# Performance work log

Measured on AMD Instinct MI355X. Metric: run time of the kernel, lower is better.

The kernel has to match this reference:

```python
import jax, jax.numpy as jnp
import numpy as np

BS, C_IN, L = 64, 64, 4096
C_OUT, KS, K, RATIO = 128, 7, 4, 4
HIDDEN = C_IN // RATIO
PAD, TEMP = 3, 30.0


def setup_inputs() -> dict:
    key = jax.random.key(0)
    k1, k2, k3, k4, k5 = jax.random.split(key, 5)
    x = jax.random.normal(k1, (BS, C_IN, L), dtype=jnp.float32)
    # attention 1x1 convs stored as matmul matrices
    w_attn1 = jax.random.normal(k2, (HIDDEN, C_IN), dtype=jnp.float32) * (2.0 / C_IN) ** 0.5
    w_attn2 = jax.random.normal(k3, (K, HIDDEN), dtype=jnp.float32) * (2.0 / HIDDEN) ** 0.5
    # K-bank conv weights [K, out, in, ks] and biases [K, out]
    weight = jax.random.normal(k4, (K, C_OUT, C_IN, KS), dtype=jnp.float32) * 0.05
    bias = jax.random.normal(k5, (K, C_OUT), dtype=jnp.float32) * 0.05
    return {"x": x, "w_attn1": w_attn1, "w_attn2": w_attn2, "weight": weight, "bias": bias}


def reference(x, w_attn1, w_attn2, weight, bias):
    # Attention1d: global avg pool -> 1x1 conv -> relu -> 1x1 conv -> softmax(./T)
    pooled = jnp.mean(x, axis=-1)                      # [bs, C_in]
    h = jax.nn.relu(pooled @ w_attn1.T)                # [bs, hidden]
    logits = h @ w_attn2.T                             # [bs, K]
    att = jax.nn.softmax(logits / TEMP, axis=-1)       # [bs, K]

    # softmax-weighted aggregation of the K weight banks -> per-sample kernels
    agg_w = jnp.einsum('bk,koif->boif', att, weight)   # [bs, out, in, ks]
    agg_b = att @ bias                                 # [bs, out]

    # per-sample conv1d (the grouped-conv trick), vectorized with vmap
    def conv_one(xi, wi):
        # xi: [C_in, L], wi: [out, in, ks]
        return jax.lax.conv_general_dilated(
            xi[None], wi, window_strides=(1,), padding=[(PAD, PAD)],
            dimension_numbers=('NCH', 'OIH', 'NCH'))[0]  # [out, L]

    out = jax.vmap(conv_one)(x, agg_w) + agg_b[:, :, None]  # [bs, out, L]
    return out
```

## Files before the change

### kernel.cpp

```cpp
#include <hip/hip_runtime.h>

typedef __bf16 bf16;
typedef __bf16 bf16x8 __attribute__((ext_vector_type(8)));
typedef __bf16 bf16x2 __attribute__((ext_vector_type(2)));
typedef float f32x4 __attribute__((ext_vector_type(4)));

#define BS 64
#define CI 64
#define LEN 4096
#define CO 128
#define KS 7
#define NK 4
#define HID 16
#define TEMP 30.0f

#define KTOT 448
#define WROW 456
#define WBAT (CO * WROW)
#define LTILE 128
#define TPB 8
#define XB_ROWS 4112
#define XB_ELE (XB_ROWS * 64)

__device__ __forceinline__ void gl_lds16(const void* g, void* l) {
    auto gp = reinterpret_cast<const __attribute__((address_space(1))) unsigned int*>(
        reinterpret_cast<unsigned long long>(g));
    auto lp = reinterpret_cast<__attribute__((address_space(3))) unsigned int*>(
        reinterpret_cast<unsigned long long>(l));
    __builtin_amdgcn_global_load_lds(gp, lp, 16, 0, 0);
}

__global__ __launch_bounds__(256) void trans_kernel(const float* __restrict__ x,
                                                    bf16* __restrict__ xbf,
                                                    float* __restrict__ part) {
    int bid = blockIdx.x;
    int b = bid >> 3, lt = bid & 7;
    int t = threadIdx.x;
    int si = t >> 2, sf = t & 3;
    __shared__ __align__(16) bf16 lds_t[128 * 72];
    __shared__ float lds_red[64 * 4];

    const float* xb = x + (size_t)b * CI * LEN;
    bf16* xo = xbf + (size_t)b * XB_ELE;
    float psum = 0.f;

    for (int st = 0; st < 4; ++st) {
        int ls = lt * 512 + st * 128;
        float4 v[8];
#pragma unroll
        for (int j = 0; j < 8; ++j)
            v[j] = *(const float4*)(xb + (size_t)si * LEN + ls + 4 * (sf + 4 * j));
#pragma unroll
        for (int j = 0; j < 8; ++j) {
            psum += (v[j].x + v[j].y) + (v[j].z + v[j].w);
#pragma unroll
            for (int e = 0; e < 4; ++e)
                lds_t[(4 * (sf + 4 * j) + e) * 72 + si] = (bf16)((&v[j].x)[e]);
        }
        __syncthreads();
        int row = t >> 4, l16 = t & 15;
#pragma unroll
        for (int pass = 0; pass < 8; ++pass) {
            int r = pass * 16 + row;
            int gl = ls + r + 8;
            uint2 d = *(const uint2*)(lds_t + r * 72 + l16 * 4);
            int c = l16 >> 1;
            int sw = c ^ (gl & 7);
            *(uint2*)((char*)xo + (size_t)gl * 128 + sw * 16 + (l16 & 1) * 8) = d;
        }
        __syncthreads();
    }

    lds_red[si * 4 + sf] = psum;
    __syncthreads();
    if (t < 64)
        part[((size_t)b * 8 + lt) * 64 + t] =
            lds_red[t * 4] + lds_red[t * 4 + 1] + lds_red[t * 4 + 2] + lds_red[t * 4 + 3];

    if (lt == 0 && t < 128) *(uint2*)((char*)xo + t * 8) = make_uint2(0u, 0u);
    if (lt == 7 && t < 128) *(uint2*)((char*)xo + (size_t)4104 * 128 + t * 8) = make_uint2(0u, 0u);
}

__global__ void aggw_kernel(const float* __restrict__ part,
                            const float* __restrict__ w1,
                            const float* __restrict__ w2,
                            const float* __restrict__ weight,
                            float* __restrict__ att_g,
                            bf16* __restrict__ wagg) {
    int o = blockIdx.x >> 1;
    int bh = blockIdx.x & 1;
    int t = threadIdx.x;
    __shared__ float p[32 * 64];
    __shared__ float hsh[32 * 16];
    __shared__ float att_s[32][4];
    __shared__ float lw[4 * KTOT];

    const float* wo = weight + (size_t)o * KTOT;
    for (int idx = t; idx < 4 * KTOT; idx += 256) {
        int bank = idx / KTOT;
        int r = idx - bank * KTOT;
        lw[idx] = wo[(size_t)bank * (CO * KTOT) + r];
    }
    for (int idx = t; idx < 32 * 64; idx += 256) {
        int bb = idx >> 6, i = idx & 63;
        const float* pp = part + ((size_t)(bh * 32 + bb) * 8) * 64 + i;
        float s = 0.f;
#pragma unroll
        for (int j = 0; j < 8; ++j) s += pp[j * 64];
        p[idx] = s * (1.0f / LEN);
    }
    __syncthreads();

    {
        int bb = t >> 3, h2 = (t & 7) * 2;
#pragma unroll
        for (int u = 0; u < 2; ++u) {
            int hh = h2 + u;
            float s = 0.f;
            for (int i = 0; i < 64; ++i) s += p[bb * 64 + i] * w1[hh * 64 + i];
            hsh[bb * 16 + hh] = fmaxf(s, 0.f);
        }
    }
    __syncthreads();
    if (t < 32) {
        float lg[NK], m = -1e30f;
#pragma unroll
        for (int k = 0; k < NK; ++k) {
            float s = 0.f;
            for (int j = 0; j < HID; ++j) s += hsh[t * 16 + j] * w2[k * HID + j];
            lg[k] = s * (1.0f / TEMP);
            m = fmaxf(m, lg[k]);
        }
        float e[NK], tot = 0.f;
#pragma unroll
        for (int k = 0; k < NK; ++k) { e[k] = expf(lg[k] - m); tot += e[k]; }
        float inv = 1.0f / tot;
#pragma unroll
        for (int k = 0; k < NK; ++k) {
            att_s[t][k] = e[k] * inv;
            if (blockIdx.x < 2) att_g[(bh * 32 + t) * NK + k] = e[k] * inv;
        }
    }
    __syncthreads();

    if (t < 224) {
        float w8[8];
#pragma unroll
        for (int j = 0; j < 2; ++j) {
            int kout = 2 * t + j;
            int i = kout & 63, f = kout >> 6;
#pragma unroll
            for (int bank = 0; bank < 4; ++bank)
                w8[j * 4 + bank] = lw[bank * KTOT + i * KS + f];
        }
        for (int bb = 0; bb < 32; ++bb) {
            int b = bh * 32 + bb;
            float a0 = att_s[bb][0], a1 = att_s[bb][1];
            float a2 = att_s[bb][2], a3 = att_s[bb][3];
            float v0 = a0 * w8[0] + a1 * w8[1] + a2 * w8[2] + a3 * w8[3];
            float v1 = a0 * w8[4] + a1 * w8[5] + a2 * w8[6] + a3 * w8[7];
            bf16x2 pk; pk[0] = (bf16)v0; pk[1] = (bf16)v1;
            *(bf16x2*)(wagg + (size_t)b * WBAT + o * WROW + 2 * t) = pk;
        }
    }
}

__global__ __launch_bounds__(256, 2) void conv_kernel(
    const bf16* __restrict__ xbf,
    const bf16* __restrict__ wagg,
    const float* __restrict__ att_g,
    const float* __restrict__ bias,
    float* __restrict__ out) {
    __shared__ __align__(1024) bf16 lds_x[2][144 * 64];
    __shared__ float aggb_l[CO];

    int nwg = gridDim.x;
    int bid = blockIdx.x;
    int logical = (bid & 7) * (nwg >> 3) + (bid >> 3);
    int b = logical >> 3;
    int rem = logical & 7;
    int oh = rem >> 2, lsp = rem & 3;

    int t = threadIdx.x;
    int lane = t & 63, wid = t >> 6;
    int ln = lane & 15, g = lane >> 4;
    int wm = wid >> 1, wn = wid & 1;

    if (t < CO) {
        float a0 = att_g[b * NK + 0], a1 = att_g[b * NK + 1];
        float a2 = att_g[b * NK + 2], a3 = att_g[b * NK + 3];
        aggb_l[t] = a0 * bias[0 * CO + t] + a1 * bias[1 * CO + t] +
                    a2 * bias[2 * CO + t] + a3 * bias[3 * CO + t];
    }

    const bf16* wgb = wagg + (size_t)b * WBAT
                    + (size_t)(oh * 64 + wm * 32 + ln) * WROW + g * 8;
    bf16x8 av[2][14];
#pragma unroll
    for (int mf = 0; mf < 2; ++mf)
#pragma unroll
        for (int kk = 0; kk < 14; ++kk)
            av[mf][kk] = *(const bf16x8*)(wgb + mf * 16 * WROW + kk * 32);

    int l0base = lsp * (LTILE * TPB);
    const bf16* xb = xbf + (size_t)b * XB_ELE;

    auto stage = [&](int buf, int l0) {
        const char* src = (const char*)xb + (size_t)l0 * 128 + lane * 16;
        char* dst = (char*)lds_x[buf];
        for (int c = wid; c < 18; c += 4)
            gl_lds16(src + c * 1024, dst + c * 1024);
    };

    stage(0, l0base);
    __syncthreads();

    float bias_r[2][4];
    int orow_off[2][4];
#pragma unroll
    for (int mf = 0; mf < 2; ++mf)
#pragma unroll
        for (int r = 0; r < 4; ++r) {
            int o = oh * 64 + wm * 32 + mf * 16 + g * 4 + r;
            bias_r[mf][r] = aggb_l[o];
            orow_off[mf][r] = (b * CO + o) * LEN;
        }

    int prow = wn * 64 + ln + 5;

    for (int tl = 0; tl < TPB; ++tl) {
        int l0 = l0base + tl * LTILE;
        if (tl + 1 < TPB) stage((tl + 1) & 1, l0 + LTILE);

        f32x4 acc[2][4];
#pragma unroll
        for (int mf = 0; mf < 2; ++mf)
#pragma unroll
            for (int nf = 0; nf < 4; ++nf)
                acc[mf][nf] = (f32x4){0.f, 0.f, 0.f, 0.f};

        const char* lb = (const char*)lds_x[tl & 1];

#pragma unroll
        for (int kk = 0; kk < 14; ++kk) {
            int f = kk >> 1;
            int key = (prow + f) & 7;
            int swz = (((kk & 1) * 4 + g) ^ key) * 16;
            bf16x8 bv[4];
#pragma unroll
            for (int nf = 0; nf < 4; ++nf)
                bv[nf] = *(const bf16x8*)(lb + (prow + nf * 16 + f) * 128 + swz);
#pragma unroll
            for (int mf = 0; mf < 2; ++mf)
#pragma unroll
                for (int nf = 0; nf < 4; ++nf)
                    acc[mf][nf] = __builtin_amdgcn_mfma_f32_16x16x32_bf16(
                        av[mf][kk], bv[nf], acc[mf][nf], 0, 0, 0);
        }

        if (tl + 1 < TPB) __syncthreads();

#pragma unroll
        for (int mf = 0; mf < 2; ++mf)
#pragma unroll
            for (int nf = 0; nf < 4; ++nf) {
                int l = l0 + wn * 64 + nf * 16 + ln;
#pragma unroll
                for (int r = 0; r < 4; ++r)
                    out[(size_t)orow_off[mf][r] + l] = acc[mf][nf][r] + bias_r[mf][r];
            }
    }
}

extern "C" void kernel_launch(void* const* d_in, const int* in_sizes, int n_in,
                              void* d_out, int out_size, void* d_ws, size_t ws_size,
                              hipStream_t stream) {
    const float* x  = (const float*)d_in[0];
    const float* w1 = (const float*)d_in[1];
    const float* w2 = (const float*)d_in[2];
    const float* wt = (const float*)d_in[3];
    const float* bs = (const float*)d_in[4];
    float* out = (float*)d_out;

    bf16* xbf    = (bf16*)d_ws;
    bf16* wagg   = (bf16*)((char*)d_ws + (size_t)BS * XB_ELE * 2);
    float* part  = (float*)((char*)wagg + (size_t)BS * WBAT * 2);
    float* att_g = part + BS * 8 * 64;

    trans_kernel<<<BS * 8, 256, 0, stream>>>(x, xbf, part);
    aggw_kernel<<<CO * 2, 256, 0, stream>>>(part, w1, w2, wt, att_g, wagg);
    conv_kernel<<<BS * 8, 256, 0, stream>>>(xbf, wagg, att_g, bs, out);
}
```

Before: 66.06 us.

## Split transpose kernel into more blocks, prefetch both tiles, widen LDS/global stores

The transpose/cast kernel now runs 16 blocks per sample instead of 8, each handling 256 columns. Both 128-column tiles are loaded into registers up front so the global reads overlap, and the LDS-to-global copy uses 16-byte vectors instead of 8-byte ones. The trailing barrier is dropped on the last tile, and the partial-sum buffer and the reduction in the aggregation kernel grow to 16 parts. The aim is more memory-level parallelism and occupancy in this bandwidth-bound pre-pass, at the cost of higher register pressure from holding 16 float4 values per thread.

Measured after the change: 66.85 us. Within noise of the previous version (+1.2%).

```diff
diff --git a/kernel.cpp b/kernel.cpp
--- a/kernel.cpp
+++ b/kernel.cpp
@@ -21,6 +21,7 @@
 #define TPB 8
 #define XB_ROWS 4112
 #define XB_ELE (XB_ROWS * 64)
+#define NPART 16
 
 __device__ __forceinline__ void gl_lds16(const void* g, void* l) {
     auto gp = reinterpret_cast<const __attribute__((address_space(1))) unsigned int*>(
@@ -34,7 +35,7 @@
                                                     bf16* __restrict__ xbf,
                                                     float* __restrict__ part) {
     int bid = blockIdx.x;
-    int b = bid >> 3, lt = bid & 7;
+    int b = bid >> 4, lt = bid & 15;
     int t = threadIdx.x;
     int si = t >> 2, sf = t & 3;
     __shared__ __align__(16) bf16 lds_t[128 * 72];
@@ -43,42 +44,49 @@
     const float* xb = x + (size_t)b * CI * LEN;
     bf16* xo = xbf + (size_t)b * XB_ELE;
     float psum = 0.f;
-
-    for (int st = 0; st < 4; ++st) {
-        int ls = lt * 512 + st * 128;
-        float4 v[8];
-#pragma unroll
-        for (int j = 0; j < 8; ++j)
-            v[j] = *(const float4*)(xb + (size_t)si * LEN + ls + 4 * (sf + 4 * j));
+    int ls0 = lt * 256;
+
+    float4 v0[8], v1[8];
+#pragma unroll
+    for (int j = 0; j < 8; ++j)
+        v0[j] = *(const float4*)(xb + (size_t)si * LEN + ls0 + 4 * (sf + 4 * j));
+#pragma unroll
+    for (int j = 0; j < 8; ++j)
+        v1[j] = *(const float4*)(xb + (size_t)si * LEN + ls0 + 128 + 4 * (sf + 4 * j));
+
+#pragma unroll
+    for (int st = 0; st < 2; ++st) {
+        const float4* v = st ? v1 : v0;
+        int ls = ls0 + st * 128;
 #pragma unroll
         for (int j = 0; j < 8; ++j) {
-            psum += (v[j].x + v[j].y) + (v[j].z + v[j].w);
+            float4 vv = v[j];
+            psum += (vv.x + vv.y) + (vv.z + vv.w);
 #pragma unroll
             for (int e = 0; e < 4; ++e)
-                lds_t[(4 * (sf + 4 * j) + e) * 72 + si] = (bf16)((&v[j].x)[e]);
+                lds_t[(4 * (sf + 4 * j) + e) * 72 + si] = (bf16)((&vv.x)[e]);
         }
         __syncthreads();
-        int row = t >> 4, l16 = t & 15;
-#pragma unroll
-        for (int pass = 0; pass < 8; ++pass) {
-            int r = pass * 16 + row;
+        int row = t >> 3, l8 = t & 7;
+#pragma unroll
+        for (int pass = 0; pass < 4; ++pass) {
+            int r = pass * 32 + row;
             int gl = ls + r + 8;
-            uint2 d = *(const uint2*)(lds_t + r * 72 + l16 * 4);
-            int c = l16 >> 1;
-            int sw = c ^ (gl & 7);
-            *(uint2*)((char*)xo + (size_t)gl * 128 + sw * 16 + (l16 & 1) * 8) = d;
-        }
-        __syncthreads();
+            uint4 d = *(const uint4*)((const char*)lds_t + r * 144 + l8 * 16);
+            int sw = l8 ^ (gl & 7);
+            *(uint4*)((char*)xo + (size_t)gl * 128 + sw * 16) = d;
+        }
+        if (st == 0) __syncthreads();
     }
 
     lds_red[si * 4 + sf] = psum;
     __syncthreads();
     if (t < 64)
-        part[((size_t)b * 8 + lt) * 64 + t] =
+        part[((size_t)b * NPART + lt) * 64 + t] =
             lds_red[t * 4] + lds_red[t * 4 + 1] + lds_red[t * 4 + 2] + lds_red[t * 4 + 3];
 
     if (lt == 0 && t < 128) *(uint2*)((char*)xo + t * 8) = make_uint2(0u, 0u);
-    if (lt == 7 && t < 128) *(uint2*)((char*)xo + (size_t)4104 * 128 + t * 8) = make_uint2(0u, 0u);
+    if (lt == 15 && t < 128) *(uint2*)((char*)xo + (size_t)4104 * 128 + t * 8) = make_uint2(0u, 0u);
 }
 
 __global__ void aggw_kernel(const float* __restrict__ part,
@@ -103,10 +111,10 @@
     }
     for (int idx = t; idx < 32 * 64; idx += 256) {
         int bb = idx >> 6, i = idx & 63;
-        const float* pp = part + ((size_t)(bh * 32 + bb) * 8) * 64 + i;
+        const float* pp = part + ((size_t)(bh * 32 + bb) * NPART) * 64 + i;
         float s = 0.f;
 #pragma unroll
-        for (int j = 0; j < 8; ++j) s += pp[j * 64];
+        for (int j = 0; j < NPART; ++j) s += pp[j * 64];
         p[idx] = s * (1.0f / LEN);
     }
     __syncthreads();
@@ -285,9 +293,9 @@
     bf16* xbf    = (bf16*)d_ws;
     bf16* wagg   = (bf16*)((char*)d_ws + (size_t)BS * XB_ELE * 2);
     float* part  = (float*)((char*)wagg + (size_t)BS * WBAT * 2);
-    float* att_g = part + BS * 8 * 64;
-
-    trans_kernel<<<BS * 8, 256, 0, stream>>>(x, xbf, part);
+    float* att_g = part + BS * NPART * 64;
+
+    trans_kernel<<<BS * 16, 256, 0, stream>>>(x, xbf, part);
     aggw_kernel<<<CO * 2, 256, 0, stream>>>(part, w1, w2, wt, att_g, wagg);
     conv_kernel<<<BS * 8, 256, 0, stream>>>(xbf, wagg, att_g, bs, out);
 }
```
